# Kernel tuning notes

Hardware: AMD Instinct MI355X
Metric: run time of the kernel (lower is better)

The kernel has to match this reference:

```python
import jax, jax.numpy as jnp
import numpy as np

EMB = 1024
NH = 16
T = 2048
B = 2

def setup_inputs() -> dict:
    key = jax.random.key(0)
    k1, k2, k3, k4, k5 = jax.random.split(key, 5)
    s = 0.02
    return {
        "x": jax.random.normal(k1, (B, T, EMB), dtype=jnp.float32),
        "W_attn": jax.random.normal(k2, (EMB, 3 * EMB), dtype=jnp.float32) * s,
        "b_attn": jax.random.normal(k3, (3 * EMB,), dtype=jnp.float32) * s,
        "W_proj": jax.random.normal(k4, (EMB, EMB), dtype=jnp.float32) * s,
        "b_proj": jax.random.normal(k5, (EMB,), dtype=jnp.float32) * s,
    }

def reference(x, W_attn, b_attn, W_proj, b_proj):
    Bz, Tz, C = x.shape
    hd = C // NH
    qkv = x @ W_attn + b_attn                      # [B,T,3C]
    q, k, v = jnp.split(qkv, 3, axis=-1)
    # [B,T,C] -> [B,H,T,hd]
    def heads(t):
        return t.reshape(Bz, Tz, NH, hd).transpose(0, 2, 1, 3)
    q, k, v = heads(q), heads(k), heads(v)
    scale = 1.0 / jnp.sqrt(jnp.float32(hd))
    att = jnp.einsum("bhqd,bhkd->bhqk", q, k) * scale   # [B,H,T,T]
    causal = jnp.tril(jnp.ones((Tz, Tz), dtype=bool))
    att = jnp.where(causal, att, jnp.finfo(att.dtype).min)
    att = jax.nn.softmax(att, axis=-1)
    y = jnp.einsum("bhqk,bhkd->bhqd", att, v)            # [B,H,T,hd]
    y = y.transpose(0, 2, 1, 3).reshape(Bz, Tz, C)
    return y @ W_proj + b_proj
```

## Files before the change

### kernel.cpp

```cpp
#include <hip/hip_runtime.h>
#include <cstdint>
#include <cstddef>

typedef _Float16 half8 __attribute__((ext_vector_type(8)));
typedef _Float16 half4v __attribute__((ext_vector_type(4)));
typedef float f32x4 __attribute__((ext_vector_type(4)));
typedef int int4v __attribute__((ext_vector_type(4)));

#define EMBD 1024
#define NHEAD 16
#define TSEQ 2048
#define NB 2
#define HD 64
#define NBH (NB*NHEAD)
#define SCK 0.18033688f

static __device__ __forceinline__ void gload_lds16(const void* g, void* l) {
    __builtin_amdgcn_global_load_lds((const __attribute__((address_space(1))) void*)g,
                                     (__attribute__((address_space(3))) void*)l,
                                     16, 0, 0);
}

static __device__ __forceinline__ int pk2(float a, float b) {
    return __builtin_bit_cast(int, __builtin_amdgcn_cvt_pkrtz(a, b));
}

__global__ void k_convert_x(const float* __restrict__ x, _Float16* __restrict__ xh, int n4) {
    int i = blockIdx.x * blockDim.x + threadIdx.x;
    if (i < n4) {
        float4 v = ((const float4*)x)[i];
        half4v h;
        h.x = (_Float16)v.x; h.y = (_Float16)v.y; h.z = (_Float16)v.z; h.w = (_Float16)v.w;
        ((half4v*)xh)[i] = h;
    }
}

__global__ void k_prep_w(const float* __restrict__ Wa, const float* __restrict__ Wp,
                         _Float16* __restrict__ WaT, _Float16* __restrict__ WpT) {
    __shared__ float tile[32][33];
    const int bx = blockIdx.x;
    const bool isA = bx < 96;
    const float* in  = isA ? Wa : Wp;
    _Float16* out    = isA ? WaT : WpT;
    const int C      = isA ? 3072 : 1024;
    const int c0 = (isA ? bx : bx - 96) * 32, r0 = blockIdx.y * 32;
    const int tx = threadIdx.x, ty = threadIdx.y;
    #pragma unroll
    for (int j = 0; j < 4; ++j)
        tile[ty + 8*j][tx] = in[(size_t)(r0 + ty + 8*j) * C + c0 + tx];
    __syncthreads();
    #pragma unroll
    for (int j = 0; j < 4; ++j)
        out[(size_t)(c0 + ty + 8*j) * 1024 + r0 + tx] = (_Float16)tile[tx][ty + 8*j];
}

__global__ __launch_bounds__(256) void k_gemm_qkv(
    const _Float16* __restrict__ A,
    const _Float16* __restrict__ Bt,
    const float* __restrict__ bias,
    _Float16* __restrict__ outq)
{
    __shared__ _Float16 As[128 * 64];
    __shared__ _Float16 Bs[128 * 64];

    const int d  = blockIdx.x;
    const int wk = (d & 7) * 96 + (d >> 3);
    const int mt = wk & 31, nt = wk >> 5;
    const int m0 = mt * 128, n0 = nt * 128;

    const int tid  = threadIdx.x;
    const int lane = tid & 63;
    const int w    = tid >> 6;
    const int wm   = w >> 1, wn = w & 1;
    const int l15  = lane & 15;
    const int lg   = lane >> 4;

    const int srow  = lane >> 3;
    const int sslot = (lane & 7) ^ srow;

    f32x4 acc[4][4];
    #pragma unroll
    for (int i = 0; i < 4; ++i)
        #pragma unroll
        for (int j = 0; j < 4; ++j)
            acc[i][j] = (f32x4){0.f, 0.f, 0.f, 0.f};

    for (int kt = 0; kt < 16; ++kt) {
        __syncthreads();
        #pragma unroll
        for (int c = 0; c < 4; ++c) {
            int r = w * 32 + c * 8 + srow;
            const _Float16* ga = A  + (size_t)(m0 + r) * 1024 + kt * 64 + sslot * 8;
            gload_lds16(ga, (char*)As + (w * 32 + c * 8) * 128);
            const _Float16* gb = Bt + (size_t)(n0 + r) * 1024 + kt * 64 + sslot * 8;
            gload_lds16(gb, (char*)Bs + (w * 32 + c * 8) * 128);
        }
        __syncthreads();

        half8 af[4][2], bf[4][2];
        #pragma unroll
        for (int mf = 0; mf < 4; ++mf) {
            int r = wm * 64 + mf * 16 + l15;
            #pragma unroll
            for (int ks = 0; ks < 2; ++ks)
                af[mf][ks] = *(const half8*)((const char*)As + r * 128 + (((ks * 4 + lg) ^ (r & 7)) * 16));
        }
        #pragma unroll
        for (int nf = 0; nf < 4; ++nf) {
            int r = wn * 64 + nf * 16 + l15;
            #pragma unroll
            for (int ks = 0; ks < 2; ++ks)
                bf[nf][ks] = *(const half8*)((const char*)Bs + r * 128 + (((ks * 4 + lg) ^ (r & 7)) * 16));
        }
        #pragma unroll
        for (int mf = 0; mf < 4; ++mf)
            #pragma unroll
            for (int nf = 0; nf < 4; ++nf) {
                acc[mf][nf] = __builtin_amdgcn_mfma_f32_16x16x32_f16(af[mf][0], bf[nf][0], acc[mf][nf], 0, 0, 0);
                acc[mf][nf] = __builtin_amdgcn_mfma_f32_16x16x32_f16(af[mf][1], bf[nf][1], acc[mf][nf], 0, 0, 0);
            }
    }

    float bv[4];
    #pragma unroll
    for (int nf = 0; nf < 4; ++nf)
        bv[nf] = bias[n0 + wn * 64 + nf * 16 + l15];
    const float osc = ((n0 >> 10) == 1) ? SCK : 1.0f;

    #pragma unroll
    for (int mf = 0; mf < 4; ++mf) {
        #pragma unroll
        for (int j = 0; j < 4; ++j) {
            int m = m0 + wm * 64 + mf * 16 + lg * 4 + j;
            _Float16* po = outq + (size_t)m * 3072 + n0 + wn * 64 + l15;
            #pragma unroll
            for (int nf = 0; nf < 4; ++nf)
                po[nf * 16] = (_Float16)((acc[mf][nf][j] + bv[nf]) * osc);
        }
    }
}

__global__ __launch_bounds__(256) void k_gemm_proj(
    const _Float16* __restrict__ A,
    const _Float16* __restrict__ Bt,
    const float* __restrict__ bias,
    float* __restrict__ outf)
{
    __shared__ _Float16 As[64 * 64];
    __shared__ _Float16 Bs[128 * 64];

    const int d  = blockIdx.x;
    const int wk = (d & 7) * 64 + (d >> 3);
    const int mt = wk & 63, nt = wk >> 6;
    const int m0 = mt * 64, n0 = nt * 128;

    const int tid  = threadIdx.x;
    const int lane = tid & 63;
    const int wn   = tid >> 6;
    const int l15  = lane & 15;
    const int lg   = lane >> 4;

    f32x4 acc[4][2];
    #pragma unroll
    for (int i = 0; i < 4; ++i) {
        acc[i][0] = (f32x4){0.f, 0.f, 0.f, 0.f};
        acc[i][1] = (f32x4){0.f, 0.f, 0.f, 0.f};
    }

    for (int kt = 0; kt < 16; ++kt) {
        __syncthreads();
        {
            #pragma unroll
            for (int c = 0; c < 2; ++c) {
                int s = c * 256 + tid;
                int r = s >> 3, sl = s & 7;
                const _Float16* ga = A + (size_t)(m0 + r) * 1024 + kt * 64 + ((sl ^ (r & 7)) * 8);
                gload_lds16(ga, (char*)As + s * 16);
            }
            #pragma unroll
            for (int c = 0; c < 4; ++c) {
                int s = c * 256 + tid;
                int r = s >> 3, sl = s & 7;
                const _Float16* gb = Bt + (size_t)(n0 + r) * 1024 + kt * 64 + ((sl ^ (r & 7)) * 8);
                gload_lds16(gb, (char*)Bs + s * 16);
            }
        }
        __syncthreads();

        half8 af[4][2], bf[2][2];
        #pragma unroll
        for (int mf = 0; mf < 4; ++mf) {
            int r = mf * 16 + l15;
            #pragma unroll
            for (int ks = 0; ks < 2; ++ks)
                af[mf][ks] = *(const half8*)((const char*)As + r * 128 + (((ks * 4 + lg) ^ (r & 7)) * 16));
        }
        #pragma unroll
        for (int nf = 0; nf < 2; ++nf) {
            int r = wn * 32 + nf * 16 + l15;
            #pragma unroll
            for (int ks = 0; ks < 2; ++ks)
                bf[nf][ks] = *(const half8*)((const char*)Bs + r * 128 + (((ks * 4 + lg) ^ (r & 7)) * 16));
        }
        #pragma unroll
        for (int mf = 0; mf < 4; ++mf)
            #pragma unroll
            for (int nf = 0; nf < 2; ++nf) {
                acc[mf][nf] = __builtin_amdgcn_mfma_f32_16x16x32_f16(af[mf][0], bf[nf][0], acc[mf][nf], 0, 0, 0);
                acc[mf][nf] = __builtin_amdgcn_mfma_f32_16x16x32_f16(af[mf][1], bf[nf][1], acc[mf][nf], 0, 0, 0);
            }
    }

    float bv[2];
    bv[0] = bias[n0 + wn * 32 + l15];
    bv[1] = bias[n0 + wn * 32 + 16 + l15];

    #pragma unroll
    for (int mf = 0; mf < 4; ++mf) {
        #pragma unroll
        for (int j = 0; j < 4; ++j) {
            int m = m0 + mf * 16 + lg * 4 + j;
            float* po = outf + (size_t)m * 1024 + n0 + wn * 32 + l15;
            po[0]  = acc[mf][0][j] + bv[0];
            po[16] = acc[mf][1][j] + bv[1];
        }
    }
}

__global__ __launch_bounds__(256) void k_vt(
    const _Float16* __restrict__ qkv,
    _Float16* __restrict__ VT)
{
    __shared__ _Float16 tile[128 * 64];

    const int tid  = threadIdx.x;
    const int tblk = blockIdx.x;
    const int bh   = blockIdx.y;
    const int b    = bh >> 4, h = bh & 15;

    {
        const int rr = tid >> 3;
        const int sl = tid & 7;
        #pragma unroll
        for (int c = 0; c < 4; ++c) {
            int r = c * 32 + rr;
            int phys = sl ^ ((r >> 4) & 7);
            const _Float16* g = qkv + (size_t)(b * 2048 + tblk * 128 + r) * 3072 + 2048 + h * 64 + sl * 8;
            *(half8*)&tile[r * 64 + phys * 8] = *(const half8*)g;
        }
    }
    __syncthreads();

    const int dd = tid >> 2;
    const int t4 = tid & 3;
    _Float16* vout = VT + ((size_t)bh * 64 + dd) * 2048 + tblk * 128 + t4 * 32;
    #pragma unroll
    for (int g = 0; g < 4; ++g) {
        half8 hv;
        #pragma unroll
        for (int e = 0; e < 8; ++e) {
            int k = 16 * (2 * t4 + (e >> 2)) + 4 * g + (e & 3);
            int phys = (dd >> 3) ^ ((k >> 4) & 7);
            hv[e] = tile[k * 64 + phys * 8 + (dd & 7)];
        }
        *(half8*)&vout[g * 8] = hv;
    }
}

__global__ __launch_bounds__(512) void k_attn(
    const _Float16* __restrict__ qkv,
    const _Float16* __restrict__ VTg,
    _Float16* __restrict__ Y)
{
    __shared__ _Float16 Kt[128 * 64];
    __shared__ _Float16 Vt[64 * 128];

    const int tid  = threadIdx.x;
    const int lane = tid & 63;
    const int w    = tid >> 6;
    const int l15  = lane & 15;
    const int lg   = lane >> 4;
    const int bh   = blockIdx.x;
    const int by   = blockIdx.y;
    const int qt   = (by < 8) ? (15 - by) : (by - 8);
    const int b    = bh >> 4, h = bh & 15;
    const size_t vbase = (size_t)bh * TSEQ * HD;

    const int rA  = tid >> 3;
    const int slA = tid & 7;
    const size_t kOffA = (size_t)rA * 3072 + ((slA ^ (rA & 7)) * 8);
    const _Float16* kBase = qkv + (size_t)(b * 2048) * 3072 + 1024 + h * 64;

    const int dA = tid >> 4;
    const int sA = tid & 15;
    const size_t vOffA = (size_t)dA * 2048 + ((sA ^ (dA & 15)) * 8);
    const _Float16* vBase = VTg + vbase;

    const int x7   = l15 & 7;
    const int kph0 = (lg ^ x7) * 8;
    const int kph1 = ((4 + lg) ^ x7) * 8;

    const int qrow = qt * 128 + w * 16 + l15;
    const _Float16* qptr = qkv + (size_t)(b * 2048 + qrow) * 3072 + h * 64;
    half8 qa0 = *(const half8*)&qptr[lg * 8];
    half8 qa1 = *(const half8*)&qptr[32 + lg * 8];

    half8 ones;
    #pragma unroll
    for (int i = 0; i < 8; ++i) ones[i] = (_Float16)1.0f;

    f32x4 yac[4];
    #pragma unroll
    for (int nf = 0; nf < 4; ++nf) yac[nf] = (f32x4){0.f, 0.f, 0.f, 0.f};
    f32x4 lsum = (f32x4){0.f, 0.f, 0.f, 0.f};

    const int nkt = qt + 1;

    half8 kra = *(const half8*)(kBase + kOffA);
    half8 krb = *(const half8*)(kBase + kOffA + (size_t)64 * 3072);
    half8 vra = *(const half8*)(vBase + vOffA);
    half8 vrb = *(const half8*)(vBase + vOffA + 32 * 2048);

    for (int kt = 0; kt < nkt; ++kt) {
        __syncthreads();
        *(half8*)&Kt[tid * 8]        = kra;
        *(half8*)&Kt[4096 + tid * 8] = krb;
        *(half8*)&Vt[tid * 8]        = vra;
        *(half8*)&Vt[4096 + tid * 8] = vrb;
        if (kt + 1 < nkt) {
            const _Float16* kp = kBase + (size_t)(kt + 1) * 128 * 3072;
            kra = *(const half8*)(kp + kOffA);
            krb = *(const half8*)(kp + kOffA + (size_t)64 * 3072);
            const _Float16* vp = vBase + (kt + 1) * 128;
            vra = *(const half8*)(vp + vOffA);
            vrb = *(const half8*)(vp + vOffA + 32 * 2048);
        }
        __syncthreads();

        const bool diag = (kt == nkt - 1);

        f32x4 s[8];
        __builtin_amdgcn_s_setprio(1);
        #pragma unroll
        for (int f = 0; f < 8; ++f) {
            if (diag && f > w) { s[f] = (f32x4){0.f, 0.f, 0.f, 0.f}; continue; }
            int rr = f * 16 + l15;
            half8 kb0 = *(const half8*)&Kt[rr * 64 + kph0];
            half8 kb1 = *(const half8*)&Kt[rr * 64 + kph1];
            f32x4 z = (f32x4){0.f, 0.f, 0.f, 0.f};
            z = __builtin_amdgcn_mfma_f32_16x16x32_f16(kb0, qa0, z, 0, 0, 0);
            z = __builtin_amdgcn_mfma_f32_16x16x32_f16(kb1, qa1, z, 0, 0, 0);
            s[f] = z;
        }
        __builtin_amdgcn_s_setprio(0);

        if (diag) {
            const int qg = qt * 128 + w * 16 + l15;
            #pragma unroll
            for (int f = 0; f < 8; ++f) {
                if (f > w) continue;
                #pragma unroll
                for (int j = 0; j < 4; ++j) {
                    int kk = kt * 128 + 16 * f + 4 * lg + j;
                    s[f][j] = (kk > qg) ? 0.f : exp2f(s[f][j]);
                }
            }
        } else {
            #pragma unroll
            for (int f = 0; f < 8; ++f)
                #pragma unroll
                for (int j = 0; j < 4; ++j) s[f][j] = exp2f(s[f][j]);
        }

        __builtin_amdgcn_s_setprio(1);
        #pragma unroll
        for (int t = 0; t < 4; ++t) {
            int4v pi;
            pi[0] = pk2(s[2 * t][0],     s[2 * t][1]);
            pi[1] = pk2(s[2 * t][2],     s[2 * t][3]);
            pi[2] = pk2(s[2 * t + 1][0], s[2 * t + 1][1]);
            pi[3] = pk2(s[2 * t + 1][2], s[2 * t + 1][3]);
            half8 pa = __builtin_bit_cast(half8, pi);
            lsum = __builtin_amdgcn_mfma_f32_16x16x32_f16(pa, ones, lsum, 0, 0, 0);
            #pragma unroll
            for (int nf = 0; nf < 4; ++nf) {
                half8 vb = *(const half8*)&Vt[(nf * 16 + l15) * 128 + (((t * 4 + lg) ^ l15) * 8)];
                yac[nf] = __builtin_amdgcn_mfma_f32_16x16x32_f16(pa, vb, yac[nf], 0, 0, 0);
            }
        }
        __builtin_amdgcn_s_setprio(0);
    }

    const int trow = qt * 128 + w * 16 + lg * 4;
    #pragma unroll
    for (int j = 0; j < 4; ++j) {
        float inv = 1.f / lsum[j];
        #pragma unroll
        for (int nf = 0; nf < 4; ++nf) {
            float yv = yac[nf][j] * inv;
            Y[((size_t)b * TSEQ + trow + j) * EMBD + h * 64 + nf * 16 + l15] = (_Float16)yv;
        }
    }
}

extern "C" void kernel_launch(void* const* d_in, const int* in_sizes, int n_in,
                              void* d_out, int out_size, void* d_ws, size_t ws_size,
                              hipStream_t stream) {
    const float* x  = (const float*)d_in[0];
    const float* Wa = (const float*)d_in[1];
    const float* ba = (const float*)d_in[2];
    const float* Wp = (const float*)d_in[3];
    const float* bp = (const float*)d_in[4];
    float* out = (float*)d_out;

    _Float16* Xh   = (_Float16*)d_ws;
    _Float16* WaT  = Xh   + (size_t)4096 * 1024;
    _Float16* WpT  = WaT  + (size_t)3072 * 1024;
    _Float16* QKVn = WpT  + (size_t)1024 * 1024;
    _Float16* VTb  = QKVn + (size_t)4096 * 3072;
    _Float16* Yh   = Xh;

    k_convert_x<<<4096, 256, 0, stream>>>(x, Xh, 1048576);
    k_prep_w<<<dim3(128, 32), dim3(32, 8), 0, stream>>>(Wa, Wp, WaT, WpT);

    k_gemm_qkv<<<768, 256, 0, stream>>>(Xh, WaT, ba, QKVn);

    k_vt<<<dim3(16, NBH), 256, 0, stream>>>(QKVn, VTb);

    k_attn<<<dim3(NBH, 16), 512, 0, stream>>>(QKVn, VTb, Yh);

    k_gemm_proj<<<512, 256, 0, stream>>>(Yh, WpT, bp, out);
}
```

Before: 105.2 us.

## Switch attention kernel to 32x32x16 MFMA with 4 waves per block

```diff
diff --git a/kernel.cpp b/kernel.cpp
--- a/kernel.cpp
+++ b/kernel.cpp
@@ -5,6 +5,7 @@
 typedef _Float16 half8 __attribute__((ext_vector_type(8)));
 typedef _Float16 half4v __attribute__((ext_vector_type(4)));
 typedef float f32x4 __attribute__((ext_vector_type(4)));
+typedef float f32x16 __attribute__((ext_vector_type(16)));
 typedef int int4v __attribute__((ext_vector_type(4)));
 
 #define EMBD 1024
@@ -169,21 +170,19 @@
 
     for (int kt = 0; kt < 16; ++kt) {
         __syncthreads();
-        {
-            #pragma unroll
-            for (int c = 0; c < 2; ++c) {
-                int s = c * 256 + tid;
-                int r = s >> 3, sl = s & 7;
-                const _Float16* ga = A + (size_t)(m0 + r) * 1024 + kt * 64 + ((sl ^ (r & 7)) * 8);
-                gload_lds16(ga, (char*)As + s * 16);
-            }
-            #pragma unroll
-            for (int c = 0; c < 4; ++c) {
-                int s = c * 256 + tid;
-                int r = s >> 3, sl = s & 7;
-                const _Float16* gb = Bt + (size_t)(n0 + r) * 1024 + kt * 64 + ((sl ^ (r & 7)) * 8);
-                gload_lds16(gb, (char*)Bs + s * 16);
-            }
+        #pragma unroll
+        for (int c = 0; c < 2; ++c) {
+            int s = c * 256 + tid;
+            int r = s >> 3, sl = s & 7;
+            const _Float16* ga = A + (size_t)(m0 + r) * 1024 + kt * 64 + ((sl ^ (r & 7)) * 8);
+            gload_lds16(ga, (char*)As + s * 16);
+        }
+        #pragma unroll
+        for (int c = 0; c < 4; ++c) {
+            int s = c * 256 + tid;
+            int r = s >> 3, sl = s & 7;
+            const _Float16* gb = Bt + (size_t)(n0 + r) * 1024 + kt * 64 + ((sl ^ (r & 7)) * 8);
+            gload_lds16(gb, (char*)Bs + s * 16);
         }
         __syncthreads();
 
@@ -259,7 +258,8 @@
         half8 hv;
         #pragma unroll
         for (int e = 0; e < 8; ++e) {
-            int k = 16 * (2 * t4 + (e >> 2)) + 4 * g + (e & 3);
+            int p = t4 * 32 + g * 8 + e;
+            int k = 16 * (p >> 4) + (p & 3) + 8 * ((p >> 2) & 1) + 4 * ((p >> 3) & 1);
             int phys = (dd >> 3) ^ ((k >> 4) & 7);
             hv[e] = tile[k * 64 + phys * 8 + (dd & 7)];
         }
@@ -267,7 +267,7 @@
     }
 }
 
-__global__ __launch_bounds__(512) void k_attn(
+__global__ __launch_bounds__(256) void k_attn(
     const _Float16* __restrict__ qkv,
     const _Float16* __restrict__ VTg,
     _Float16* __restrict__ Y)
@@ -278,128 +278,131 @@
     const int tid  = threadIdx.x;
     const int lane = tid & 63;
     const int w    = tid >> 6;
-    const int l15  = lane & 15;
-    const int lg   = lane >> 4;
+    const int l31  = lane & 31;
+    const int hi   = lane >> 5;
     const int bh   = blockIdx.x;
     const int by   = blockIdx.y;
     const int qt   = (by < 8) ? (15 - by) : (by - 8);
     const int b    = bh >> 4, h = bh & 15;
-    const size_t vbase = (size_t)bh * TSEQ * HD;
-
-    const int rA  = tid >> 3;
-    const int slA = tid & 7;
-    const size_t kOffA = (size_t)rA * 3072 + ((slA ^ (rA & 7)) * 8);
+
+    int koff[4], voff[4];
+    #pragma unroll
+    for (int c = 0; c < 4; ++c) {
+        int seg = c * 256 + tid;
+        int r = seg >> 3, sl = seg & 7;
+        koff[c] = r * 3072 + ((sl ^ (r & 7)) * 8);
+        int d2 = seg >> 4, s16 = seg & 15;
+        voff[c] = d2 * 2048 + ((s16 ^ (d2 & 15)) * 8);
+    }
     const _Float16* kBase = qkv + (size_t)(b * 2048) * 3072 + 1024 + h * 64;
-
-    const int dA = tid >> 4;
-    const int sA = tid & 15;
-    const size_t vOffA = (size_t)dA * 2048 + ((sA ^ (dA & 15)) * 8);
-    const _Float16* vBase = VTg + vbase;
-
-    const int x7   = l15 & 7;
-    const int kph0 = (lg ^ x7) * 8;
-    const int kph1 = ((4 + lg) ^ x7) * 8;
-
-    const int qrow = qt * 128 + w * 16 + l15;
+    const _Float16* vBase = VTg + (size_t)bh * TSEQ * HD;
+
+    const int qrow = qt * 128 + w * 32 + l31;
     const _Float16* qptr = qkv + (size_t)(b * 2048 + qrow) * 3072 + h * 64;
-    half8 qa0 = *(const half8*)&qptr[lg * 8];
-    half8 qa1 = *(const half8*)&qptr[32 + lg * 8];
-
-    half8 ones;
-    #pragma unroll
-    for (int i = 0; i < 8; ++i) ones[i] = (_Float16)1.0f;
-
-    f32x4 yac[4];
-    #pragma unroll
-    for (int nf = 0; nf < 4; ++nf) yac[nf] = (f32x4){0.f, 0.f, 0.f, 0.f};
-    f32x4 lsum = (f32x4){0.f, 0.f, 0.f, 0.f};
+    half8 qb[4];
+    #pragma unroll
+    for (int v = 0; v < 4; ++v)
+        qb[v] = *(const half8*)&qptr[16 * v + 8 * hi];
+
+    f32x16 yac0, yac1;
+    #pragma unroll
+    for (int r = 0; r < 16; ++r) { yac0[r] = 0.f; yac1[r] = 0.f; }
+    float lsum = 0.f;
 
     const int nkt = qt + 1;
 
-    half8 kra = *(const half8*)(kBase + kOffA);
-    half8 krb = *(const half8*)(kBase + kOffA + (size_t)64 * 3072);
-    half8 vra = *(const half8*)(vBase + vOffA);
-    half8 vrb = *(const half8*)(vBase + vOffA + 32 * 2048);
+    half8 kr[4], vr[4];
+    #pragma unroll
+    for (int c = 0; c < 4; ++c) {
+        kr[c] = *(const half8*)(kBase + koff[c]);
+        vr[c] = *(const half8*)(vBase + voff[c]);
+    }
 
     for (int kt = 0; kt < nkt; ++kt) {
         __syncthreads();
-        *(half8*)&Kt[tid * 8]        = kra;
-        *(half8*)&Kt[4096 + tid * 8] = krb;
-        *(half8*)&Vt[tid * 8]        = vra;
-        *(half8*)&Vt[4096 + tid * 8] = vrb;
+        #pragma unroll
+        for (int c = 0; c < 4; ++c) {
+            *(half8*)&Kt[(c * 256 + tid) * 8] = kr[c];
+            *(half8*)&Vt[(c * 256 + tid) * 8] = vr[c];
+        }
         if (kt + 1 < nkt) {
             const _Float16* kp = kBase + (size_t)(kt + 1) * 128 * 3072;
-            kra = *(const half8*)(kp + kOffA);
-            krb = *(const half8*)(kp + kOffA + (size_t)64 * 3072);
             const _Float16* vp = vBase + (kt + 1) * 128;
-            vra = *(const half8*)(vp + vOffA);
-            vrb = *(const half8*)(vp + vOffA + 32 * 2048);
+            #pragma unroll
+            for (int c = 0; c < 4; ++c) {
+                kr[c] = *(const half8*)(kp + koff[c]);
+                vr[c] = *(const half8*)(vp + voff[c]);
+            }
         }
         __syncthreads();
 
         const bool diag = (kt == nkt - 1);
-
-        f32x4 s[8];
-        __builtin_amdgcn_s_setprio(1);
-        #pragma unroll
-        for (int f = 0; f < 8; ++f) {
-            if (diag && f > w) { s[f] = (f32x4){0.f, 0.f, 0.f, 0.f}; continue; }
-            int rr = f * 16 + l15;
-            half8 kb0 = *(const half8*)&Kt[rr * 64 + kph0];
-            half8 kb1 = *(const half8*)&Kt[rr * 64 + kph1];
-            f32x4 z = (f32x4){0.f, 0.f, 0.f, 0.f};
-            z = __builtin_amdgcn_mfma_f32_16x16x32_f16(kb0, qa0, z, 0, 0, 0);
-            z = __builtin_amdgcn_mfma_f32_16x16x32_f16(kb1, qa1, z, 0, 0, 0);
-            s[f] = z;
-        }
-        __builtin_amdgcn_s_setprio(0);
-
-        if (diag) {
-            const int qg = qt * 128 + w * 16 + l15;
-            #pragma unroll
-            for (int f = 0; f < 8; ++f) {
-                if (f > w) continue;
+        const int x7  = l31 & 7;
+        const int x15 = l31 & 15;
+
+        #pragma unroll
+        for (int t = 0; t < 4; ++t) {
+            if (diag && t > w) continue;
+
+            f32x16 s;
+            #pragma unroll
+            for (int r = 0; r < 16; ++r) s[r] = 0.f;
+            __builtin_amdgcn_s_setprio(1);
+            #pragma unroll
+            for (int v = 0; v < 4; ++v) {
+                half8 kb = *(const half8*)&Kt[(32 * t + l31) * 64 + (((2 * v + hi) ^ x7) * 8)];
+                s = __builtin_amdgcn_mfma_f32_32x32x16_f16(kb, qb[v], s, 0, 0, 0);
+            }
+            __builtin_amdgcn_s_setprio(0);
+
+            if (diag && t == w) {
+                const int qg = qt * 128 + w * 32 + l31;
+                const int kb0 = kt * 128 + 32 * t;
                 #pragma unroll
-                for (int j = 0; j < 4; ++j) {
-                    int kk = kt * 128 + 16 * f + 4 * lg + j;
-                    s[f][j] = (kk > qg) ? 0.f : exp2f(s[f][j]);
+                for (int r = 0; r < 16; ++r) {
+                    int kk = kb0 + (r & 3) + 8 * (r >> 2) + 4 * hi;
+                    float p = (kk > qg) ? 0.f : exp2f(s[r]);
+                    s[r] = p;
+                    lsum += p;
                 }
-            }
-        } else {
-            #pragma unroll
-            for (int f = 0; f < 8; ++f)
+            } else {
                 #pragma unroll
-                for (int j = 0; j < 4; ++j) s[f][j] = exp2f(s[f][j]);
-        }
-
-        __builtin_amdgcn_s_setprio(1);
-        #pragma unroll
-        for (int t = 0; t < 4; ++t) {
-            int4v pi;
-            pi[0] = pk2(s[2 * t][0],     s[2 * t][1]);
-            pi[1] = pk2(s[2 * t][2],     s[2 * t][3]);
-            pi[2] = pk2(s[2 * t + 1][0], s[2 * t + 1][1]);
-            pi[3] = pk2(s[2 * t + 1][2], s[2 * t + 1][3]);
-            half8 pa = __builtin_bit_cast(half8, pi);
-            lsum = __builtin_amdgcn_mfma_f32_16x16x32_f16(pa, ones, lsum, 0, 0, 0);
-            #pragma unroll
-            for (int nf = 0; nf < 4; ++nf) {
-                half8 vb = *(const half8*)&Vt[(nf * 16 + l15) * 128 + (((t * 4 + lg) ^ l15) * 8)];
-                yac[nf] = __builtin_amdgcn_mfma_f32_16x16x32_f16(pa, vb, yac[nf], 0, 0, 0);
-            }
-        }
-        __builtin_amdgcn_s_setprio(0);
-    }
-
-    const int trow = qt * 128 + w * 16 + lg * 4;
-    #pragma unroll
-    for (int j = 0; j < 4; ++j) {
-        float inv = 1.f / lsum[j];
-        #pragma unroll
-        for (int nf = 0; nf < 4; ++nf) {
-            float yv = yac[nf][j] * inv;
-            Y[((size_t)b * TSEQ + trow + j) * EMBD + h * 64 + nf * 16 + l15] = (_Float16)yv;
-        }
+                for (int r = 0; r < 16; ++r) {
+                    float p = exp2f(s[r]);
+                    s[r] = p;
+                    lsum += p;
+                }
+            }
+
+            __builtin_amdgcn_s_setprio(1);
+            #pragma unroll
+            for (int half = 0; half < 2; ++half) {
+                int4v pi;
+                pi[0] = pk2(s[8 * half + 0], s[8 * half + 1]);
+                pi[1] = pk2(s[8 * half + 2], s[8 * half + 3]);
+                pi[2] = pk2(s[8 * half + 4], s[8 * half + 5]);
+                pi[3] = pk2(s[8 * half + 6], s[8 * half + 7]);
+                half8 pa = __builtin_bit_cast(half8, pi);
+                int slot = 2 * (2 * t + half) + hi;
+                half8 vb0 = *(const half8*)&Vt[l31 * 128        + ((slot ^ x15) * 8)];
+                half8 vb1 = *(const half8*)&Vt[(32 + l31) * 128 + ((slot ^ x15) * 8)];
+                yac0 = __builtin_amdgcn_mfma_f32_32x32x16_f16(pa, vb0, yac0, 0, 0, 0);
+                yac1 = __builtin_amdgcn_mfma_f32_32x32x16_f16(pa, vb1, yac1, 0, 0, 0);
+            }
+            __builtin_amdgcn_s_setprio(0);
+        }
+    }
+
+    lsum += __shfl_xor(lsum, 32);
+
+    const int trow = qt * 128 + w * 32;
+    #pragma unroll
+    for (int r = 0; r < 16; ++r) {
+        int ql = (r & 3) + 8 * (r >> 2) + 4 * hi;
+        float inv = 1.0f / __shfl(lsum, ql);
+        _Float16* po = Y + ((size_t)b * TSEQ + trow + ql) * EMBD + h * 64 + l31;
+        po[0]  = (_Float16)(yac0[r] * inv);
+        po[32] = (_Float16)(yac1[r] * inv);
     }
 }
 
@@ -427,7 +430,7 @@
 
     k_vt<<<dim3(16, NBH), 256, 0, stream>>>(QKVn, VTb);
 
-    k_attn<<<dim3(NBH, 16), 512, 0, stream>>>(QKVn, VTb, Yh);
+    k_attn<<<dim3(NBH, 16), 256, 0, stream>>>(QKVn, VTb, Yh);
 
     k_gemm_proj<<<512, 256, 0, stream>>>(Yh, WpT, bp, out);
 }
```

New measurement: 115.2 us. +9.5%, slower.
